# Optimization experiments

Hardware: AMD Instinct MI355X
Metric: run time of the kernel (lower is better)

## Reference

```python
import jax, jax.numpy as jnp
import numpy as np

N = 262144   # total elems in batch
C = 65536    # total reactions in batch
E = 200      # orig_elem_fea_len
R = 128      # orig_reaction_fea_len
H = 4        # n_heads
DIMS = [E + R, 256, 256, 256, 256, 128, 128, 64]  # input + embed_dims
RES_LAYERS = (0, 4, 6)  # layers where dims[i] != dims[i+1] -> Linear residual


def setup_inputs() -> dict:
    key = jax.random.key(0)
    ks = jax.random.split(key, 64)
    inp = {}
    inp["orig_elem_fea"] = jax.random.normal(ks[0], (N, E), jnp.float32)
    inp["reaction_elem_idx"] = jax.random.randint(ks[1], (N,), 0, C, dtype=jnp.int32)
    inp["reaction_embed"] = jax.random.normal(ks[2], (C, R), jnp.float32)
    for i in range(7):
        din, dout = DIMS[i], DIMS[i + 1]
        inp[f"w{i}"] = jax.random.normal(ks[3 + i], (H, dout, din), jnp.float32) / np.float32(np.sqrt(din))
        inp[f"b{i}"] = jnp.zeros((H, dout), jnp.float32)
    for j, i in enumerate(RES_LAYERS):
        din, dout = DIMS[i], DIMS[i + 1]
        inp[f"rw{i}"] = jax.random.normal(ks[12 + j], (H, dout, din), jnp.float32) / np.float32(np.sqrt(din))
    inp["wout"] = jax.random.normal(ks[20], (H, 1, DIMS[-1]), jnp.float32) / np.float32(np.sqrt(DIMS[-1]))
    inp["bout"] = jnp.zeros((H, 1), jnp.float32)
    return inp


def _stoich_forward(orig_elem_fea, reaction_elem_idx, reaction_embed,
                    ws, bs, rws, wout, bout):
    # gather reaction embedding per elem + concat  -> (N, E+R)
    fea = jnp.concatenate([orig_elem_fea, reaction_embed[reaction_elem_idx]], axis=1)
    # per-head ResidualNetwork, vectorized across heads via leading H axis
    h = None  # (H, N, d)
    for i in range(7):
        if i == 0:
            z = jnp.einsum('hoi,ni->hno', ws[0], fea)
            res = jnp.einsum('hoi,ni->hno', rws[0], fea)
        else:
            z = jnp.einsum('hoi,hni->hno', ws[i], h)
            res = jnp.einsum('hoi,hni->hno', rws[i], h) if i in rws else h
        h = jax.nn.relu(z + bs[i][:, None, :]) + res
    gate = (jnp.einsum('hoi,hni->hno', wout, h) + bout[:, None, :])[..., 0]  # (H, N)
    # segment softmax over reactions (per head)
    g = gate.T  # (N, H)
    idx = reaction_elem_idx
    m = jax.ops.segment_max(g, idx, num_segments=C)          # (C, H)
    e = jnp.exp(g - m[idx])
    denom = jax.ops.segment_sum(e, idx, num_segments=C)[idx] + 1e-13
    stoich = e / denom                                       # (N, H)
    return stoich.mean(axis=1)                               # (N,)


def reference(orig_elem_fea, reaction_elem_idx, reaction_embed,
              w0, b0, w1, b1, w2, b2, w3, b3, w4, b4, w5, b5, w6, b6,
              rw0, rw4, rw6, wout, bout):
    ws = [w0, w1, w2, w3, w4, w5, w6]
    bs = [b0, b1, b2, b3, b4, b5, b6]
    rws = {0: rw0, 4: rw4, 6: rw6}
    return _stoich_forward(orig_elem_fea, reaction_elem_idx, reaction_embed,
                           ws, bs, rws, wout, bout)
```

## Files before the change

### kernel.cpp

```cpp
#include <hip/hip_runtime.h>


constexpr int NN  = 262144;
constexpr int CC  = 65536;
constexpr int TM  = 64;
constexpr int BLK = 256;

typedef _Float16 f16x8 __attribute__((ext_vector_type(8)));
typedef float    f32x4 __attribute__((ext_vector_type(4)));

constexpr size_t OFF_W0  = 0;
constexpr size_t OFF_RW0 = 360448;
constexpr size_t OFF_W1  = 720896;
constexpr size_t OFF_W2  = 983040;
constexpr size_t OFF_W3  = 1245184;
constexpr size_t OFF_W4  = 1507328;
constexpr size_t OFF_RW4 = 1638400;
constexpr size_t OFF_W5  = 1769472;
constexpr size_t OFF_W6  = 1835008;
constexpr size_t OFF_RW6 = 1867776;
constexpr size_t HSTRIDE = 1900544;

__device__ __forceinline__ unsigned fenc(float f) {
  unsigned u = __float_as_uint(f);
  return (u & 0x80000000u) ? ~u : (u | 0x80000000u);
}
__device__ __forceinline__ float fdec(unsigned u) {
  return (u & 0x80000000u) ? __uint_as_float(u & 0x7fffffffu)
                           : __uint_as_float(~u);
}

__global__ __launch_bounds__(256) void pack_kernel(
    const float* __restrict__ w0, const float* __restrict__ rw0,
    const float* __restrict__ w1, const float* __restrict__ w2,
    const float* __restrict__ w3, const float* __restrict__ w4,
    const float* __restrict__ rw4, const float* __restrict__ w5,
    const float* __restrict__ w6, const float* __restrict__ rw6,
    char* __restrict__ packed)
{
  const int job = blockIdx.y, head = blockIdx.z;
  const float* src; int DIN, DOUT, NK; size_t off;
  switch (job) {
    case 0: src = w0;  DIN = 328; DOUT = 256; NK = 11; off = OFF_W0;  break;
    case 1: src = rw0; DIN = 328; DOUT = 256; NK = 11; off = OFF_RW0; break;
    case 2: src = w1;  DIN = 256; DOUT = 256; NK = 8;  off = OFF_W1;  break;
    case 3: src = w2;  DIN = 256; DOUT = 256; NK = 8;  off = OFF_W2;  break;
    case 4: src = w3;  DIN = 256; DOUT = 256; NK = 8;  off = OFF_W3;  break;
    case 5: src = w4;  DIN = 256; DOUT = 128; NK = 8;  off = OFF_W4;  break;
    case 6: src = rw4; DIN = 256; DOUT = 128; NK = 8;  off = OFF_RW4; break;
    case 7: src = w5;  DIN = 128; DOUT = 128; NK = 4;  off = OFF_W5;  break;
    case 8: src = w6;  DIN = 128; DOUT = 64;  NK = 4;  off = OFF_W6;  break;
    default: src = rw6; DIN = 128; DOUT = 64; NK = 4;  off = OFF_RW6; break;
  }
  const int nct = DOUT >> 4;
  const int tid = blockIdx.x * 256 + threadIdx.x;
  if (tid >= nct * NK * 64) return;
  const int l = tid & 63, fs = tid >> 6;
  const int ks = fs % NK, ct = fs / NK;
  const int o  = ct * 16 + (l & 15);
  const int kb = ks * 32 + (l >> 4) * 8;
  float a[8];
  if (kb < DIN) {
    const float* p = src + (size_t)head * DOUT * DIN + (size_t)o * DIN + kb;
#pragma unroll
    for (int j = 0; j < 8; ++j) a[j] = p[j];
  } else {
#pragma unroll
    for (int j = 0; j < 8; ++j) a[j] = 0.f;
  }
  f16x8 hi, lo;
#pragma unroll
  for (int j = 0; j < 8; ++j) {
    _Float16 h = (_Float16)a[j];
    hi[j] = h;
    lo[j] = (_Float16)(a[j] - (float)h);
  }
  char* dst = packed + (size_t)head * HSTRIDE + off + (size_t)fs * 2048 + l * 16;
  *(f16x8*)dst = hi;
  *(f16x8*)(dst + 1024) = lo;
}

__device__ __forceinline__ void stage_chunk(const char* src, char* dst) {
  __builtin_amdgcn_global_load_lds(
      (const __attribute__((address_space(1))) unsigned int*)src,
      (__attribute__((address_space(3))) unsigned int*)dst, 16, 0, 0);
}

template<int NCT, int NK>
__device__ __forceinline__ void stage_ks(const char* packB, char* dst,
                                         int ks, int lane, int wv) {
  constexpr int CH = NCT * 2;
#pragma unroll
  for (int j = 0; j < CH / 4; ++j) {
    const int i  = j * 4 + wv;
    const int ct = i >> 1, p = i & 1;
    const char* src = packB + (size_t)(ct * NK + ks) * 2048 + p * 1024 + (size_t)lane * 16;
    stage_chunk(src, dst + i * 1024);
  }
}

template<bool GA>
__device__ __forceinline__ void load_a(
    const float* actw, const float* orig, const float* embed,
    int n, int e, int ks, int lane, f16x8& Ah, f16x8& Al)
{
  float a[8];
  if constexpr (GA) {
    const int q = lane >> 4;
    const int g = ks * 4 + q;
    if (g <= 24) {
      const float* p = orig + (size_t)n * 200 + g * 8;
#pragma unroll
      for (int j = 0; j < 8; ++j) a[j] = p[j];
    } else if (g <= 40) {
      const float* p = embed + (size_t)e * 128 + (g - 25) * 8;
#pragma unroll
      for (int j = 0; j < 8; ++j) a[j] = p[j];
    } else {
#pragma unroll
      for (int j = 0; j < 8; ++j) a[j] = 0.f;
    }
  } else {
    const int m  = lane & 15;
    const int c0 = ks * 8 + (lane >> 4) * 2;
    const int i0 = m * 256 + ((c0 ^ (m & 7)) << 2);
    f32x4 x0 = *(const f32x4*)(actw + i0);
    f32x4 x1 = *(const f32x4*)(actw + (i0 ^ 4));
    a[0] = x0[0]; a[1] = x0[1]; a[2] = x0[2]; a[3] = x0[3];
    a[4] = x1[0]; a[5] = x1[1]; a[6] = x1[2]; a[7] = x1[3];
  }
#pragma unroll
  for (int j = 0; j < 8; ++j) {
    _Float16 h = (_Float16)a[j];
    Ah[j] = h;
    Al[j] = (_Float16)(a[j] - (float)h);
  }
}

template<int NCT, int NK, bool GA>
__device__ __forceinline__ void sweep(
    const char* packB, const float* actw, char* stg,
    const float* orig, const float* embed, int n, int e,
    int lane, int wv, f32x4 acc[NCT])
{
  stage_ks<NCT, NK>(packB, stg, 0, lane, wv);
  __syncthreads();
  int buf = 0;
  for (int ks = 0; ks < NK; ++ks) {
    if (ks + 1 < NK)
      stage_ks<NCT, NK>(packB, stg + (buf ^ 1) * 32768, ks + 1, lane, wv);
    f16x8 Ah, Al;
    load_a<GA>(actw, orig, embed, n, e, ks, lane, Ah, Al);
    const char* base = stg + buf * 32768;
#pragma unroll
    for (int ct = 0; ct < NCT; ++ct) {
      const char* f = base + ct * 2048 + lane * 16;
      f16x8 Bh = *(const f16x8*)f;
      f16x8 Bl = *(const f16x8*)(f + 1024);
      acc[ct] = __builtin_amdgcn_mfma_f32_16x16x32_f16(Ah, Bh, acc[ct], 0, 0, 0);
      acc[ct] = __builtin_amdgcn_mfma_f32_16x16x32_f16(Ah, Bl, acc[ct], 0, 0, 0);
      acc[ct] = __builtin_amdgcn_mfma_f32_16x16x32_f16(Al, Bh, acc[ct], 0, 0, 0);
    }
    __syncthreads();
    buf ^= 1;
  }
}

template<int NCT, bool RW>
__device__ __forceinline__ void epilogue(
    f32x4 acc[NCT], f32x4 accr[NCT], const float* bias,
    float* actw, int lane)
{
#pragma unroll
  for (int ct = 0; ct < NCT; ++ct) {
    const int col = ct * 16 + (lane & 15);
    const float b = bias[col];
#pragma unroll
    for (int jr = 0; jr < 4; ++jr) {
      const int row = (lane >> 4) * 4 + jr;
      const int fi  = row * 256 + (((col >> 2) ^ (row & 7)) << 2) + (col & 3);
      float v = fmaxf(acc[ct][jr] + b, 0.f);
      if (RW) v += accr[ct][jr];
      else    v += actw[fi];
      actw[fi] = v;
    }
  }
}

__global__ __launch_bounds__(BLK, 1) void mlp_kernel(
    const float* __restrict__ orig, const int* __restrict__ ridx,
    const float* __restrict__ embed, const char* __restrict__ packed,
    const float* __restrict__ b0, const float* __restrict__ b1,
    const float* __restrict__ b2, const float* __restrict__ b3,
    const float* __restrict__ b4, const float* __restrict__ b5,
    const float* __restrict__ b6,
    const float* __restrict__ wout, const float* __restrict__ bout,
    float* __restrict__ gate, unsigned* __restrict__ mmax)
{
  extern __shared__ char smem[];
  float* act = (float*)smem;
  char*  stg = smem + 65536;
  const int t    = threadIdx.x;
  const int lane = t & 63;
  const int wv   = t >> 6;
  const int n0   = blockIdx.x * TM;
  float* actw = act + wv * (16 * 256);
  const int m = lane & 15, q = lane >> 4;
  const int n = n0 + wv * 16 + m;
  const int e = ridx[n];
  const f32x4 Z4 = {0.f, 0.f, 0.f, 0.f};

  for (int head = 0; head < 4; ++head) {
    const char* pk = packed + (size_t)head * HSTRIDE;
    {
      f32x4 accr[16], acc[16];
#pragma unroll
      for (int i = 0; i < 16; ++i) { accr[i] = Z4; acc[i] = Z4; }
      sweep<16, 11, true>(pk + OFF_RW0, actw, stg, orig, embed, n, e, lane, wv, accr);
      sweep<16, 11, true>(pk + OFF_W0,  actw, stg, orig, embed, n, e, lane, wv, acc);
      epilogue<16, true>(acc, accr, b0 + head * 256, actw, lane);
    }
    {
      f32x4 acc[16];
#pragma unroll
      for (int i = 0; i < 16; ++i) acc[i] = Z4;
      sweep<16, 8, false>(pk + OFF_W1, actw, stg, orig, embed, n, e, lane, wv, acc);
      epilogue<16, false>(acc, acc, b1 + head * 256, actw, lane);
    }
    {
      f32x4 acc[16];
#pragma unroll
      for (int i = 0; i < 16; ++i) acc[i] = Z4;
      sweep<16, 8, false>(pk + OFF_W2, actw, stg, orig, embed, n, e, lane, wv, acc);
      epilogue<16, false>(acc, acc, b2 + head * 256, actw, lane);
    }
    {
      f32x4 acc[16];
#pragma unroll
      for (int i = 0; i < 16; ++i) acc[i] = Z4;
      sweep<16, 8, false>(pk + OFF_W3, actw, stg, orig, embed, n, e, lane, wv, acc);
      epilogue<16, false>(acc, acc, b3 + head * 256, actw, lane);
    }
    {
      f32x4 accr[8], acc[8];
#pragma unroll
      for (int i = 0; i < 8; ++i) { accr[i] = Z4; acc[i] = Z4; }
      sweep<8, 8, false>(pk + OFF_RW4, actw, stg, orig, embed, n, e, lane, wv, accr);
      sweep<8, 8, false>(pk + OFF_W4,  actw, stg, orig, embed, n, e, lane, wv, acc);
      epilogue<8, true>(acc, accr, b4 + head * 128, actw, lane);
    }
    {
      f32x4 acc[8];
#pragma unroll
      for (int i = 0; i < 8; ++i) acc[i] = Z4;
      sweep<8, 4, false>(pk + OFF_W5, actw, stg, orig, embed, n, e, lane, wv, acc);
      epilogue<8, false>(acc, acc, b5 + head * 128, actw, lane);
    }
    {
      f32x4 accr[4], acc[4];
#pragma unroll
      for (int i = 0; i < 4; ++i) { accr[i] = Z4; acc[i] = Z4; }
      sweep<4, 4, false>(pk + OFF_RW6, actw, stg, orig, embed, n, e, lane, wv, accr);
      sweep<4, 4, false>(pk + OFF_W6,  actw, stg, orig, embed, n, e, lane, wv, acc);
      float g[4] = {0.f, 0.f, 0.f, 0.f};
#pragma unroll
      for (int ct = 0; ct < 4; ++ct) {
        const int col = ct * 16 + m;
        const float bb = b6[head * 64 + col];
        const float wo = wout[head * 64 + col];
#pragma unroll
        for (int jr = 0; jr < 4; ++jr) {
          float v = fmaxf(acc[ct][jr] + bb, 0.f) + accr[ct][jr];
          g[jr] += v * wo;
        }
      }
#pragma unroll
      for (int jr = 0; jr < 4; ++jr) {
        g[jr] += __shfl_xor(g[jr], 1);
        g[jr] += __shfl_xor(g[jr], 2);
        g[jr] += __shfl_xor(g[jr], 4);
        g[jr] += __shfl_xor(g[jr], 8);
      }
      if (m == 0) {
        const float bo = bout[head];
#pragma unroll
        for (int jr = 0; jr < 4; ++jr) {
          const int nn = n0 + wv * 16 + q * 4 + jr;
          const float gg = g[jr] + bo;
          gate[(size_t)nn * 4 + head] = gg;
          atomicMax(mmax + (size_t)ridx[nn] * 4 + head, fenc(gg));
        }
      }
    }
  }
}

__global__ __launch_bounds__(BLK) void sm_pass2(
    const int* __restrict__ ridx, const unsigned* __restrict__ mmax,
    float* __restrict__ gate, float* __restrict__ denom)
{
  int tt = blockIdx.x * BLK + threadIdx.x;
  int n = tt >> 2, h = tt & 3;
  float g = gate[tt];
  int c = ridx[n];
  float mm = fdec(mmax[(size_t)c * 4 + h]);
  float ev = expf(g - mm);
  gate[tt] = ev;
  atomicAdd(denom + (size_t)c * 4 + h, ev);
}

__global__ __launch_bounds__(BLK) void sm_finalize(
    const int* __restrict__ ridx, const float* __restrict__ gate,
    const float* __restrict__ denom, float* __restrict__ out)
{
  int n = blockIdx.x * BLK + threadIdx.x;
  float4 e4 = *(const float4*)(gate + (size_t)n * 4);
  int c = ridx[n];
  float4 d4 = *(const float4*)(denom + (size_t)c * 4);
  out[n] = 0.25f * (e4.x / (d4.x + 1e-13f) + e4.y / (d4.y + 1e-13f) +
                    e4.z / (d4.z + 1e-13f) + e4.w / (d4.w + 1e-13f));
}

extern "C" void kernel_launch(void* const* d_in, const int* in_sizes, int n_in,
                              void* d_out, int out_size, void* d_ws, size_t ws_size,
                              hipStream_t stream) {
  (void)in_sizes; (void)n_in; (void)out_size; (void)ws_size;
  const float* orig  = (const float*)d_in[0];
  const int*   ridx  = (const int*)d_in[1];
  const float* embed = (const float*)d_in[2];
  const float* w0 = (const float*)d_in[3];  const float* b0 = (const float*)d_in[4];
  const float* w1 = (const float*)d_in[5];  const float* b1 = (const float*)d_in[6];
  const float* w2 = (const float*)d_in[7];  const float* b2 = (const float*)d_in[8];
  const float* w3 = (const float*)d_in[9];  const float* b3 = (const float*)d_in[10];
  const float* w4 = (const float*)d_in[11]; const float* b4 = (const float*)d_in[12];
  const float* w5 = (const float*)d_in[13]; const float* b5 = (const float*)d_in[14];
  const float* w6 = (const float*)d_in[15]; const float* b6 = (const float*)d_in[16];
  const float* rw0 = (const float*)d_in[17];
  const float* rw4 = (const float*)d_in[18];
  const float* rw6 = (const float*)d_in[19];
  const float* wout = (const float*)d_in[20];
  const float* bout = (const float*)d_in[21];

  float*    gate   = (float*)d_ws;
  unsigned* mmax   = (unsigned*)((char*)d_ws + (size_t)4 * 1024 * 1024);
  float*    denom  = (float*)((char*)d_ws + (size_t)5 * 1024 * 1024);
  char*     packed = (char*)d_ws + (size_t)6 * 1024 * 1024;

  hipMemsetAsync(mmax, 0, (size_t)CC * 4 * sizeof(unsigned), stream);
  hipMemsetAsync(denom, 0, (size_t)CC * 4 * sizeof(float), stream);

  pack_kernel<<<dim3(44, 10, 4), 256, 0, stream>>>(
      w0, rw0, w1, w2, w3, w4, rw4, w5, w6, rw6, packed);

  hipFuncSetAttribute((const void*)mlp_kernel,
                      hipFuncAttributeMaxDynamicSharedMemorySize, 131072);
  mlp_kernel<<<NN / TM, BLK, 131072, stream>>>(
      orig, ridx, embed, packed,
      b0, b1, b2, b3, b4, b5, b6, wout, bout, gate, mmax);

  sm_pass2<<<NN * 4 / BLK, BLK, 0, stream>>>(ridx, mmax, gate, denom);
  sm_finalize<<<NN / BLK, BLK, 0, stream>>>(ridx, gate, denom, (float*)d_out);
}
```

Measured before the change: 5.915 ms.

## Split output columns across waves, read weights from global, store activations as fp16 hi/lo

Each wave now covers all 64 rows of the tile but only a quarter of the output columns. B fragments are loaded straight from global/L2 instead of being staged into LDS with double buffering. Activations are kept in LDS as pre-split fp16 hi/lo pairs, which removes the per-k conversion and halves LDS use so two blocks can share a CU. The gate reduction now goes through a small LDS partial buffer. The trade-off is more block-wide barriers, B reads that depend on cache hit rate, and higher register pressure from the 4x4 accumulator arrays.

```diff
diff --git a/kernel.cpp b/kernel.cpp
--- a/kernel.cpp
+++ b/kernel.cpp
@@ -80,114 +80,102 @@
   *(f16x8*)(dst + 1024) = lo;
 }
 
-__device__ __forceinline__ void stage_chunk(const char* src, char* dst) {
-  __builtin_amdgcn_global_load_lds(
-      (const __attribute__((address_space(1))) unsigned int*)src,
-      (__attribute__((address_space(3))) unsigned int*)dst, 16, 0, 0);
-}
-
-template<int NCT, int NK>
-__device__ __forceinline__ void stage_ks(const char* packB, char* dst,
-                                         int ks, int lane, int wv) {
-  constexpr int CH = NCT * 2;
-#pragma unroll
-  for (int j = 0; j < CH / 4; ++j) {
-    const int i  = j * 4 + wv;
-    const int ct = i >> 1, p = i & 1;
-    const char* src = packB + (size_t)(ct * NK + ks) * 2048 + p * 1024 + (size_t)lane * 16;
-    stage_chunk(src, dst + i * 1024);
-  }
-}
-
-template<bool GA>
-__device__ __forceinline__ void load_a(
-    const float* actw, const float* orig, const float* embed,
-    int n, int e, int ks, int lane, f16x8& Ah, f16x8& Al)
-{
-  float a[8];
-  if constexpr (GA) {
-    const int q = lane >> 4;
-    const int g = ks * 4 + q;
-    if (g <= 24) {
-      const float* p = orig + (size_t)n * 200 + g * 8;
-#pragma unroll
-      for (int j = 0; j < 8; ++j) a[j] = p[j];
-    } else if (g <= 40) {
-      const float* p = embed + (size_t)e * 128 + (g - 25) * 8;
-#pragma unroll
-      for (int j = 0; j < 8; ++j) a[j] = p[j];
-    } else {
-#pragma unroll
-      for (int j = 0; j < 8; ++j) a[j] = 0.f;
-    }
-  } else {
-    const int m  = lane & 15;
-    const int c0 = ks * 8 + (lane >> 4) * 2;
-    const int i0 = m * 256 + ((c0 ^ (m & 7)) << 2);
-    f32x4 x0 = *(const f32x4*)(actw + i0);
-    f32x4 x1 = *(const f32x4*)(actw + (i0 ^ 4));
-    a[0] = x0[0]; a[1] = x0[1]; a[2] = x0[2]; a[3] = x0[3];
-    a[4] = x1[0]; a[5] = x1[1]; a[6] = x1[2]; a[7] = x1[3];
-  }
-#pragma unroll
-  for (int j = 0; j < 8; ++j) {
-    _Float16 h = (_Float16)a[j];
-    Ah[j] = h;
-    Al[j] = (_Float16)(a[j] - (float)h);
-  }
+#define MFMA16(A, B, C) __builtin_amdgcn_mfma_f32_16x16x32_f16((A), (B), (C), 0, 0, 0)
+
+__device__ __forceinline__ int aoff(int row, int chunk) {
+  return (row * 32 + (chunk ^ (row & 7))) * 16;
 }
 
 template<int NCT, int NK, bool GA>
 __device__ __forceinline__ void sweep(
-    const char* packB, const float* actw, char* stg,
-    const float* orig, const float* embed, int n, int e,
-    int lane, int wv, f32x4 acc[NCT])
-{
-  stage_ks<NCT, NK>(packB, stg, 0, lane, wv);
-  __syncthreads();
-  int buf = 0;
+    const char* __restrict__ packB,
+    const char* __restrict__ aH, const char* __restrict__ aL,
+    const float* __restrict__ orig, const float* __restrict__ embed,
+    const int* nrt, const int* ert,
+    int lane, int wv, f32x4 acc[NCT / 4][4])
+{
+  constexpr int W = NCT / 4;
+  const int m = lane & 15, q = lane >> 4;
+#pragma unroll
   for (int ks = 0; ks < NK; ++ks) {
-    if (ks + 1 < NK)
-      stage_ks<NCT, NK>(packB, stg + (buf ^ 1) * 32768, ks + 1, lane, wv);
-    f16x8 Ah, Al;
-    load_a<GA>(actw, orig, embed, n, e, ks, lane, Ah, Al);
-    const char* base = stg + buf * 32768;
-#pragma unroll
-    for (int ct = 0; ct < NCT; ++ct) {
-      const char* f = base + ct * 2048 + lane * 16;
-      f16x8 Bh = *(const f16x8*)f;
-      f16x8 Bl = *(const f16x8*)(f + 1024);
-      acc[ct] = __builtin_amdgcn_mfma_f32_16x16x32_f16(Ah, Bh, acc[ct], 0, 0, 0);
-      acc[ct] = __builtin_amdgcn_mfma_f32_16x16x32_f16(Ah, Bl, acc[ct], 0, 0, 0);
-      acc[ct] = __builtin_amdgcn_mfma_f32_16x16x32_f16(Al, Bh, acc[ct], 0, 0, 0);
-    }
-    __syncthreads();
-    buf ^= 1;
-  }
-}
-
-template<int NCT, bool RW>
+    f16x8 Ah[4], Al[4];
+#pragma unroll
+    for (int rt = 0; rt < 4; ++rt) {
+      if constexpr (GA) {
+        const int g = ks * 4 + q;
+        float a[8];
+        if (g <= 24) {
+          const float* p = orig + (size_t)nrt[rt] * 200 + g * 8;
+#pragma unroll
+          for (int j = 0; j < 8; ++j) a[j] = p[j];
+        } else if (g <= 40) {
+          const float* p = embed + (size_t)ert[rt] * 128 + (g - 25) * 8;
+#pragma unroll
+          for (int j = 0; j < 8; ++j) a[j] = p[j];
+        } else {
+#pragma unroll
+          for (int j = 0; j < 8; ++j) a[j] = 0.f;
+        }
+#pragma unroll
+        for (int j = 0; j < 8; ++j) {
+          _Float16 h = (_Float16)a[j];
+          Ah[rt][j] = h;
+          Al[rt][j] = (_Float16)(a[j] - (float)h);
+        }
+      } else {
+        const int off = aoff(rt * 16 + m, ks * 4 + q);
+        Ah[rt] = *(const f16x8*)(aH + off);
+        Al[rt] = *(const f16x8*)(aL + off);
+      }
+    }
+#pragma unroll
+    for (int i = 0; i < W; ++i) {
+      const char* f = packB + (size_t)((wv + i * 4) * NK + ks) * 2048 + lane * 16;
+      const f16x8 Bh = *(const f16x8*)f;
+      const f16x8 Bl = *(const f16x8*)(f + 1024);
+#pragma unroll
+      for (int rt = 0; rt < 4; ++rt) {
+        acc[i][rt] = MFMA16(Ah[rt], Bh, acc[i][rt]);
+        acc[i][rt] = MFMA16(Ah[rt], Bl, acc[i][rt]);
+        acc[i][rt] = MFMA16(Al[rt], Bh, acc[i][rt]);
+      }
+    }
+  }
+}
+
+template<int W, int MODE>
 __device__ __forceinline__ void epilogue(
-    f32x4 acc[NCT], f32x4 accr[NCT], const float* bias,
-    float* actw, int lane)
-{
-#pragma unroll
-  for (int ct = 0; ct < NCT; ++ct) {
-    const int col = ct * 16 + (lane & 15);
-    const float b = bias[col];
-#pragma unroll
-    for (int jr = 0; jr < 4; ++jr) {
-      const int row = (lane >> 4) * 4 + jr;
-      const int fi  = row * 256 + (((col >> 2) ^ (row & 7)) << 2) + (col & 3);
-      float v = fmaxf(acc[ct][jr] + b, 0.f);
-      if (RW) v += accr[ct][jr];
-      else    v += actw[fi];
-      actw[fi] = v;
-    }
-  }
-}
-
-__global__ __launch_bounds__(BLK, 1) void mlp_kernel(
+    f32x4 acc[W][4], f32x4 accr[W][4], const float* __restrict__ bias,
+    char* aH, char* aL, int lane, int wv)
+{
+  const int m = lane & 15, q = lane >> 4;
+#pragma unroll
+  for (int i = 0; i < W; ++i) {
+    const int col = (wv + i * 4) * 16 + m;
+    const float b = (MODE == 1) ? 0.f : bias[col];
+    const int cchunk = col >> 3, csub = (col & 7) * 2;
+#pragma unroll
+    for (int rt = 0; rt < 4; ++rt) {
+#pragma unroll
+      for (int jr = 0; jr < 4; ++jr) {
+        const int row = rt * 16 + q * 4 + jr;
+        const int off = aoff(row, cchunk) + csub;
+        _Float16* ph = (_Float16*)(aH + off);
+        _Float16* pl = (_Float16*)(aL + off);
+        float v;
+        if constexpr (MODE == 0)      v = fmaxf(acc[i][rt][jr] + b, 0.f);
+        else if constexpr (MODE == 1) v = ((float)*ph + (float)*pl) + accr[i][rt][jr];
+        else if constexpr (MODE == 2) v = fmaxf(acc[i][rt][jr] + b, 0.f) + ((float)*ph + (float)*pl);
+        else                          v = fmaxf(acc[i][rt][jr] + b, 0.f) + accr[i][rt][jr];
+        _Float16 h = (_Float16)v;
+        *ph = h;
+        *pl = (_Float16)(v - (float)h);
+      }
+    }
+  }
+}
+
+__global__ __launch_bounds__(BLK, 2) void mlp_kernel(
     const float* __restrict__ orig, const int* __restrict__ ridx,
     const float* __restrict__ embed, const char* __restrict__ packed,
     const float* __restrict__ b0, const float* __restrict__ b1,
@@ -198,99 +186,127 @@
     float* __restrict__ gate, unsigned* __restrict__ mmax)
 {
   extern __shared__ char smem[];
-  float* act = (float*)smem;
-  char*  stg = smem + 65536;
-  const int t    = threadIdx.x;
-  const int lane = t & 63;
-  const int wv   = t >> 6;
-  const int n0   = blockIdx.x * TM;
-  float* actw = act + wv * (16 * 256);
+  char*  aH    = smem;
+  char*  aL    = smem + 32768;
+  float* gpart = (float*)(smem + 65536);
+  const int t = threadIdx.x, lane = t & 63, wv = t >> 6;
   const int m = lane & 15, q = lane >> 4;
-  const int n = n0 + wv * 16 + m;
-  const int e = ridx[n];
+  const int n0 = blockIdx.x * TM;
+  int nrt[4], ert[4];
+#pragma unroll
+  for (int rt = 0; rt < 4; ++rt) {
+    nrt[rt] = n0 + rt * 16 + m;
+    ert[rt] = ridx[nrt[rt]];
+  }
   const f32x4 Z4 = {0.f, 0.f, 0.f, 0.f};
 
+#pragma unroll 1
   for (int head = 0; head < 4; ++head) {
     const char* pk = packed + (size_t)head * HSTRIDE;
     {
-      f32x4 accr[16], acc[16];
-#pragma unroll
-      for (int i = 0; i < 16; ++i) { accr[i] = Z4; acc[i] = Z4; }
-      sweep<16, 11, true>(pk + OFF_RW0, actw, stg, orig, embed, n, e, lane, wv, accr);
-      sweep<16, 11, true>(pk + OFF_W0,  actw, stg, orig, embed, n, e, lane, wv, acc);
-      epilogue<16, true>(acc, accr, b0 + head * 256, actw, lane);
-    }
-    {
-      f32x4 acc[16];
-#pragma unroll
-      for (int i = 0; i < 16; ++i) acc[i] = Z4;
-      sweep<16, 8, false>(pk + OFF_W1, actw, stg, orig, embed, n, e, lane, wv, acc);
-      epilogue<16, false>(acc, acc, b1 + head * 256, actw, lane);
-    }
-    {
-      f32x4 acc[16];
-#pragma unroll
-      for (int i = 0; i < 16; ++i) acc[i] = Z4;
-      sweep<16, 8, false>(pk + OFF_W2, actw, stg, orig, embed, n, e, lane, wv, acc);
-      epilogue<16, false>(acc, acc, b2 + head * 256, actw, lane);
-    }
-    {
-      f32x4 acc[16];
-#pragma unroll
-      for (int i = 0; i < 16; ++i) acc[i] = Z4;
-      sweep<16, 8, false>(pk + OFF_W3, actw, stg, orig, embed, n, e, lane, wv, acc);
-      epilogue<16, false>(acc, acc, b3 + head * 256, actw, lane);
-    }
-    {
-      f32x4 accr[8], acc[8];
-#pragma unroll
-      for (int i = 0; i < 8; ++i) { accr[i] = Z4; acc[i] = Z4; }
-      sweep<8, 8, false>(pk + OFF_RW4, actw, stg, orig, embed, n, e, lane, wv, accr);
-      sweep<8, 8, false>(pk + OFF_W4,  actw, stg, orig, embed, n, e, lane, wv, acc);
-      epilogue<8, true>(acc, accr, b4 + head * 128, actw, lane);
-    }
-    {
-      f32x4 acc[8];
-#pragma unroll
-      for (int i = 0; i < 8; ++i) acc[i] = Z4;
-      sweep<8, 4, false>(pk + OFF_W5, actw, stg, orig, embed, n, e, lane, wv, acc);
-      epilogue<8, false>(acc, acc, b5 + head * 128, actw, lane);
-    }
-    {
-      f32x4 accr[4], acc[4];
-#pragma unroll
-      for (int i = 0; i < 4; ++i) { accr[i] = Z4; acc[i] = Z4; }
-      sweep<4, 4, false>(pk + OFF_RW6, actw, stg, orig, embed, n, e, lane, wv, accr);
-      sweep<4, 4, false>(pk + OFF_W6,  actw, stg, orig, embed, n, e, lane, wv, acc);
-      float g[4] = {0.f, 0.f, 0.f, 0.f};
-#pragma unroll
-      for (int ct = 0; ct < 4; ++ct) {
-        const int col = ct * 16 + m;
-        const float bb = b6[head * 64 + col];
-        const float wo = wout[head * 64 + col];
+      f32x4 acc[4][4];
+#pragma unroll
+      for (int i = 0; i < 4; ++i)
+#pragma unroll
+        for (int r = 0; r < 4; ++r) acc[i][r] = Z4;
+      sweep<16, 11, true>(pk + OFF_W0, aH, aL, orig, embed, nrt, ert, lane, wv, acc);
+      epilogue<4, 0>(acc, acc, b0 + head * 256, aH, aL, lane, wv);
+#pragma unroll
+      for (int i = 0; i < 4; ++i)
+#pragma unroll
+        for (int r = 0; r < 4; ++r) acc[i][r] = Z4;
+      sweep<16, 11, true>(pk + OFF_RW0, aH, aL, orig, embed, nrt, ert, lane, wv, acc);
+      epilogue<4, 1>(acc, acc, b0 + head * 256, aH, aL, lane, wv);
+      __syncthreads();
+    }
+    {
+      f32x4 acc[4][4];
+#pragma unroll
+      for (int i = 0; i < 4; ++i)
+#pragma unroll
+        for (int r = 0; r < 4; ++r) acc[i][r] = Z4;
+      sweep<16, 8, false>(pk + OFF_W1, aH, aL, orig, embed, nrt, ert, lane, wv, acc);
+      __syncthreads();
+      epilogue<4, 2>(acc, acc, b1 + head * 256, aH, aL, lane, wv);
+      __syncthreads();
+    }
+    {
+      f32x4 acc[4][4];
+#pragma unroll
+      for (int i = 0; i < 4; ++i)
+#pragma unroll
+        for (int r = 0; r < 4; ++r) acc[i][r] = Z4;
+      sweep<16, 8, false>(pk + OFF_W2, aH, aL, orig, embed, nrt, ert, lane, wv, acc);
+      __syncthreads();
+      epilogue<4, 2>(acc, acc, b2 + head * 256, aH, aL, lane, wv);
+      __syncthreads();
+    }
+    {
+      f32x4 acc[4][4];
+#pragma unroll
+      for (int i = 0; i < 4; ++i)
+#pragma unroll
+        for (int r = 0; r < 4; ++r) acc[i][r] = Z4;
+      sweep<16, 8, false>(pk + OFF_W3, aH, aL, orig, embed, nrt, ert, lane, wv, acc);
+      __syncthreads();
+      epilogue<4, 2>(acc, acc, b3 + head * 256, aH, aL, lane, wv);
+      __syncthreads();
+    }
+    {
+      f32x4 acc[2][4], accr[2][4];
+#pragma unroll
+      for (int i = 0; i < 2; ++i)
+#pragma unroll
+        for (int r = 0; r < 4; ++r) { acc[i][r] = Z4; accr[i][r] = Z4; }
+      sweep<8, 8, false>(pk + OFF_W4,  aH, aL, orig, embed, nrt, ert, lane, wv, acc);
+      sweep<8, 8, false>(pk + OFF_RW4, aH, aL, orig, embed, nrt, ert, lane, wv, accr);
+      __syncthreads();
+      epilogue<2, 3>(acc, accr, b4 + head * 128, aH, aL, lane, wv);
+      __syncthreads();
+    }
+    {
+      f32x4 acc[2][4];
+#pragma unroll
+      for (int i = 0; i < 2; ++i)
+#pragma unroll
+        for (int r = 0; r < 4; ++r) acc[i][r] = Z4;
+      sweep<8, 4, false>(pk + OFF_W5, aH, aL, orig, embed, nrt, ert, lane, wv, acc);
+      __syncthreads();
+      epilogue<2, 2>(acc, acc, b5 + head * 128, aH, aL, lane, wv);
+      __syncthreads();
+    }
+    {
+      f32x4 acc[1][4], accr[1][4];
+#pragma unroll
+      for (int r = 0; r < 4; ++r) { acc[0][r] = Z4; accr[0][r] = Z4; }
+      sweep<4, 4, false>(pk + OFF_W6,  aH, aL, orig, embed, nrt, ert, lane, wv, acc);
+      sweep<4, 4, false>(pk + OFF_RW6, aH, aL, orig, embed, nrt, ert, lane, wv, accr);
+      __syncthreads();
+      const int col = wv * 16 + m;
+      const float bb = b6[head * 64 + col];
+      const float wo = wout[head * 64 + col];
+#pragma unroll
+      for (int rt = 0; rt < 4; ++rt) {
 #pragma unroll
         for (int jr = 0; jr < 4; ++jr) {
-          float v = fmaxf(acc[ct][jr] + bb, 0.f) + accr[ct][jr];
-          g[jr] += v * wo;
+          float v = fmaxf(acc[0][rt][jr] + bb, 0.f) + accr[0][rt][jr];
+          float p = v * wo;
+          p += __shfl_xor(p, 1);
+          p += __shfl_xor(p, 2);
+          p += __shfl_xor(p, 4);
+          p += __shfl_xor(p, 8);
+          if (m == 0) gpart[wv * 64 + rt * 16 + q * 4 + jr] = p;
         }
       }
-#pragma unroll
-      for (int jr = 0; jr < 4; ++jr) {
-        g[jr] += __shfl_xor(g[jr], 1);
-        g[jr] += __shfl_xor(g[jr], 2);
-        g[jr] += __shfl_xor(g[jr], 4);
-        g[jr] += __shfl_xor(g[jr], 8);
-      }
-      if (m == 0) {
-        const float bo = bout[head];
-#pragma unroll
-        for (int jr = 0; jr < 4; ++jr) {
-          const int nn = n0 + wv * 16 + q * 4 + jr;
-          const float gg = g[jr] + bo;
-          gate[(size_t)nn * 4 + head] = gg;
-          atomicMax(mmax + (size_t)ridx[nn] * 4 + head, fenc(gg));
-        }
-      }
+      __syncthreads();
+      if (t < 64) {
+        float g = gpart[t] + gpart[64 + t] + gpart[128 + t] + gpart[192 + t]
+                + bout[head];
+        const int n = n0 + t;
+        gate[(size_t)n * 4 + head] = g;
+        atomicMax(mmax + (size_t)ridx[n] * 4 + head, fenc(g));
+      }
+      __syncthreads();
     }
   }
 }
@@ -353,8 +369,8 @@
       w0, rw0, w1, w2, w3, w4, rw4, w5, w6, rw6, packed);
 
   hipFuncSetAttribute((const void*)mlp_kernel,
-                      hipFuncAttributeMaxDynamicSharedMemorySize, 131072);
-  mlp_kernel<<<NN / TM, BLK, 131072, stream>>>(
+                      hipFuncAttributeMaxDynamicSharedMemorySize, 66560);
+  mlp_kernel<<<NN / TM, BLK, 66560, stream>>>(
       orig, ridx, embed, packed,
       b0, b1, b2, b3, b4, b5, b6, wout, bout, gate, mmax);
 
```

Result: slower. 6.810 ms (+15.1%).
